# Optimization experiments

Measured on AMD Instinct MI355X. Metric: run time of the kernel, lower is better.

The kernel has to match this reference:

```python
import jax, jax.numpy as jnp
import numpy as np

N_NODES = 50000
N_EDGES = 800000
IN_DIM = 128
HID_DIM = 128
N_CLASSES = 40


def setup_inputs() -> dict:
    key = jax.random.key(0)
    ks = jax.random.split(key, 12)
    s = 0.05
    inp = {
        "X": jax.random.normal(ks[0], (N_NODES, IN_DIM), jnp.float32),
        "A": jax.random.randint(ks[1], (2, N_EDGES), 0, N_NODES, dtype=jnp.int64),
        "W0": jax.random.normal(ks[2], (HID_DIM, IN_DIM), jnp.float32) * s,
        "b0": jnp.zeros((HID_DIM,), jnp.float32),
        "W1": jax.random.normal(ks[3], (HID_DIM, HID_DIM), jnp.float32) * s,
        "b1": jnp.zeros((HID_DIM,), jnp.float32),
        "W2": jax.random.normal(ks[4], (HID_DIM, HID_DIM), jnp.float32) * s,
        "b2": jnp.zeros((HID_DIM,), jnp.float32),
        "W3": jax.random.normal(ks[5], (HID_DIM, HID_DIM), jnp.float32) * s,
        "b3": jnp.zeros((HID_DIM,), jnp.float32),
        "Wf": jax.random.normal(ks[6], (N_CLASSES, HID_DIM), jnp.float32) * s,
        "bf": jnp.zeros((N_CLASSES,), jnp.float32),
    }
    return inp


def _gcn_conv(x, W, b, src, dst):
    # FrobeniusNormGCNConv: normalize weight by Frobenius norm, then standard GCNConv
    Wn = W / jnp.linalg.norm(W)
    h = x @ Wn.T  # [N, out]
    # gcn_norm with self-loops (edge weight 1.0): deg over targets + 1 self loop
    ones = jnp.ones((dst.shape[0],), h.dtype)
    deg = jax.ops.segment_sum(ones, dst, num_segments=N_NODES) + 1.0
    dinv = jax.lax.rsqrt(deg)  # [N]
    norm = dinv[src] * dinv[dst]  # [E]
    # scatter-add of normalized source messages into targets
    agg = jax.ops.segment_sum(norm[:, None] * h[src], dst, num_segments=N_NODES)
    # self-loop contribution: dinv[i]^2 * h[i]; bias added after aggregation
    return agg + (dinv * dinv)[:, None] * h + b


def reference(X, A, W0, b0, W1, b1, W2, b2, W3, b3, Wf, bf):
    src, dst = A[0], A[1]
    h = _gcn_conv(X, W0, b0, src, dst)
    skip = h
    for W, b in ((W1, b1), (W2, b2), (W3, b3)):
        h = _gcn_conv(h, W, b, src, dst)
        h = jax.nn.relu(h)
        h = h + skip  # residual skip (dropout identity in eval mode)
        skip = h
    return h @ Wf.T + bf
```

## Files before the change

### kernel.cpp

```cpp
#include <hip/hip_runtime.h>

#define N_NODES_C 50000
#define N_EDGES_C 800000
#define DIM 128
#define NCLS 40
#define NBUK 32
#define BCAP 32768
#define NOCT 16

typedef __attribute__((ext_vector_type(8))) short bf16x8;
typedef __attribute__((ext_vector_type(4))) float f32x4;

__device__ inline float bf2f(unsigned short u) {
    union { unsigned int i; float f; } c;
    c.i = ((unsigned int)u) << 16;
    return c.f;
}
__device__ inline unsigned short f2bf(float f) {
    union { float f; unsigned int i; } c;
    c.f = f;
    unsigned int x = c.i;
    x += 0x7fffu + ((x >> 16) & 1u);
    return (unsigned short)(x >> 16);
}
__device__ inline void unp8(const uint4& g, float* f) {
    f[0] = __uint_as_float(g.x << 16); f[1] = __uint_as_float(g.x & 0xFFFF0000u);
    f[2] = __uint_as_float(g.y << 16); f[3] = __uint_as_float(g.y & 0xFFFF0000u);
    f[4] = __uint_as_float(g.z << 16); f[5] = __uint_as_float(g.z & 0xFFFF0000u);
    f[6] = __uint_as_float(g.w << 16); f[7] = __uint_as_float(g.w & 0xFFFF0000u);
}

__global__ __launch_bounds__(256) void k_pre(const float* __restrict__ W0,
                                             const float* __restrict__ W1,
                                             const float* __restrict__ W2,
                                             const float* __restrict__ W3,
                                             const float* __restrict__ Wf,
                                             unsigned short* __restrict__ Wb,
                                             unsigned short* __restrict__ Wfb,
                                             float* __restrict__ scale_inv,
                                             int* __restrict__ gcount) {
    int b = blockIdx.x;
    if (b < 64) {
        int m = b >> 4;
        int idx = (b & 15) * 256 + threadIdx.x;
        const float* W = m == 0 ? W0 : m == 1 ? W1 : m == 2 ? W2 : W3;
        float4 v = reinterpret_cast<const float4*>(W)[idx];
        reinterpret_cast<ushort4*>(Wb + (size_t)m * DIM * DIM)[idx] =
            make_ushort4(f2bf(v.x), f2bf(v.y), f2bf(v.z), f2bf(v.w));
        return;
    }
    b -= 64;
    if (b < 5) {
        int idx = b * 256 + threadIdx.x;
        float4 v = reinterpret_cast<const float4*>(Wf)[idx];
        reinterpret_cast<ushort4*>(Wfb)[idx] =
            make_ushort4(f2bf(v.x), f2bf(v.y), f2bf(v.z), f2bf(v.w));
        return;
    }
    b -= 5;
    if (b == 0 && threadIdx.x < NBUK) gcount[threadIdx.x] = 0;
    const float* W = b == 0 ? W0 : b == 1 ? W1 : b == 2 ? W2 : W3;
    float s = 0.f;
    for (int i = threadIdx.x; i < DIM * DIM; i += 256) {
        float v = W[i];
        s += v * v;
    }
    #pragma unroll
    for (int off = 32; off >= 1; off >>= 1) s += __shfl_down(s, off);
    __shared__ float red[4];
    int lane = threadIdx.x & 63, wid = threadIdx.x >> 6;
    if (lane == 0) red[wid] = s;
    __syncthreads();
    if (threadIdx.x == 0) {
        float tot = red[0] + red[1] + red[2] + red[3];
        scale_inv[b] = 1.0f / sqrtf(tot);
    }
}

__global__ __launch_bounds__(256) void k_bucket(const int* __restrict__ A,
                                                int* __restrict__ gcount,
                                                unsigned int* __restrict__ ebuk, int E) {
    __shared__ int cnt[NBUK];
    __shared__ int gbase[NBUK];
    int tid = threadIdx.x;
    if (tid < NBUK) cnt[tid] = 0;
    __syncthreads();
    int e0 = blockIdx.x * 1024;
    int s[4], d[4], b[4], r[4];
    #pragma unroll
    for (int j = 0; j < 4; ++j) {
        int e = e0 + j * 256 + tid;
        if (e < E) {
            s[j] = A[e];
            d[j] = A[E + e];
            b[j] = (int)(((unsigned long long)(unsigned)d[j] * NBUK) / N_NODES_C);
            r[j] = atomicAdd(&cnt[b[j]], 1);
        } else {
            b[j] = -1;
        }
    }
    __syncthreads();
    if (tid < NBUK) gbase[tid] = atomicAdd(&gcount[tid], cnt[tid]);
    __syncthreads();
    #pragma unroll
    for (int j = 0; j < 4; ++j) {
        if (b[j] >= 0) {
            int pos = gbase[b[j]] + r[j];
            if (pos < BCAP)
                ebuk[(size_t)b[j] * BCAP + pos] =
                    ((unsigned)d[j] << 16) | (unsigned)s[j];
        }
    }
}

__global__ __launch_bounds__(512) void k_csr(const unsigned int* __restrict__ ebuk,
                                             const int* __restrict__ gcount,
                                             int* __restrict__ ptr,
                                             float* __restrict__ dinv,
                                             unsigned short* __restrict__ esrc) {
    __shared__ unsigned int dlo[NOCT / 2][1568];
    __shared__ int gc[NBUK];
    __shared__ int wsum2[8], wpre2[8];
    int k = blockIdx.x;
    int tid = threadIdx.x;
    int base = (k * N_NODES_C + NBUK - 1) / NBUK;
    int next = ((k + 1) * N_NODES_C + NBUK - 1) / NBUK;
    int sz = next - base;

    for (int i = tid; i < (NOCT / 2) * 1568; i += 512) (&dlo[0][0])[i] = 0;
    if (tid < NBUK) gc[tid] = min(gcount[tid], BCAP);
    __syncthreads();

    int count = gc[k];
    int bucket_base = 0;
    #pragma unroll
    for (int j = 0; j < NBUK; ++j) bucket_base += (j < k) ? gc[j] : 0;
    const unsigned int* eb = ebuk + (size_t)k * BCAP;

    for (int i = tid; i < count; i += 512) {
        unsigned v = eb[i];
        int d = (int)(v >> 16) - base;
        int src = (int)(v & 0xFFFFu);
        int oct = (src * NOCT) / N_NODES_C;
        atomicAdd(&dlo[oct >> 1][d], 1u << ((oct & 1) * 16));
    }
    __syncthreads();

    int degloc[4];
    int mysum = 0;
    #pragma unroll
    for (int c = 0; c < 4; ++c) {
        int i = tid * 4 + c;
        int ds = 0;
        if (i < sz) {
            #pragma unroll
            for (int p = 0; p < NOCT / 2; ++p) {
                unsigned v = dlo[p][i];
                ds += (int)(v & 0xFFFFu) + (int)(v >> 16);
            }
        }
        degloc[c] = ds;
        mysum += ds;
    }
    int lane = tid & 63, wid = tid >> 6;
    int sc = mysum;
    #pragma unroll
    for (int off = 1; off < 64; off <<= 1) {
        int t = __shfl_up(sc, off);
        if (lane >= off) sc += t;
    }
    if (lane == 63) wsum2[wid] = sc;
    __syncthreads();
    if (tid == 0) {
        int a = 0;
        #pragma unroll
        for (int w = 0; w < 8; ++w) { wpre2[w] = a; a += wsum2[w]; }
    }
    __syncthreads();
    int run = wpre2[wid] + sc - mysum;
    #pragma unroll
    for (int c = 0; c < 4; ++c) {
        int i = tid * 4 + c;
        if (i < sz) {
            ptr[base + i] = bucket_base + run;
            dinv[base + i] = rsqrtf((float)degloc[c] + 1.0f);
            int r = run;
            #pragma unroll
            for (int p = 0; p < NOCT / 2; ++p) {
                unsigned v = dlo[p][i];
                int lo = (int)(v & 0xFFFFu), hi = (int)(v >> 16);
                dlo[p][i] = (unsigned)r | ((unsigned)(r + lo) << 16);
                r += lo + hi;
            }
            run += degloc[c];
        }
    }
    if (k == NBUK - 1 && tid == 511) ptr[N_NODES_C] = bucket_base + run;
    __syncthreads();

    for (int i = tid; i < count; i += 512) {
        unsigned v = eb[i];
        int d = (int)(v >> 16) - base;
        int src = (int)(v & 0xFFFFu);
        int oct = (src * NOCT) / N_NODES_C;
        unsigned old = atomicAdd(&dlo[oct >> 1][d], 1u << ((oct & 1) * 16));
        int pos = (int)((old >> ((oct & 1) * 16)) & 0xFFFFu);
        esrc[bucket_base + pos] = (unsigned short)src;
    }
}

template <bool F32A>
__global__ __launch_bounds__(256) void k_gemm_mfma(const void* __restrict__ Xp,
                                                   const unsigned short* __restrict__ Wb,
                                                   const float* __restrict__ scale_ptr,
                                                   const float* __restrict__ dinv,
                                                   unsigned short* __restrict__ Gb, int N) {
    int tid = threadIdx.x;
    int w = tid >> 6;
    int l = tid & 63;
    int l15 = l & 15;
    int lg = l >> 4;
    int arow = blockIdx.x * 64 + w * 16 + l15;
    if (arow >= N) arow = N - 1;
    float scale = scale_ptr[0];

    f32x4 acc[8];
    #pragma unroll
    for (int ct = 0; ct < 8; ++ct) acc[ct] = f32x4{0.f, 0.f, 0.f, 0.f};

    #pragma unroll
    for (int kc = 0; kc < 4; ++kc) {
        int ko = kc * 32 + lg * 8;
        bf16x8 a;
        if (F32A) {
            const float4* xf = reinterpret_cast<const float4*>(
                (const float*)Xp + (size_t)arow * DIM + ko);
            float4 u = xf[0], v = xf[1];
            a[0] = (short)f2bf(u.x); a[1] = (short)f2bf(u.y);
            a[2] = (short)f2bf(u.z); a[3] = (short)f2bf(u.w);
            a[4] = (short)f2bf(v.x); a[5] = (short)f2bf(v.y);
            a[6] = (short)f2bf(v.z); a[7] = (short)f2bf(v.w);
        } else {
            a = *reinterpret_cast<const bf16x8*>(
                (const unsigned short*)Xp + (size_t)arow * DIM + ko);
        }
        #pragma unroll
        for (int ct = 0; ct < 8; ++ct) {
            bf16x8 b = *reinterpret_cast<const bf16x8*>(&Wb[(size_t)(ct * 16 + l15) * DIM + ko]);
            acc[ct] = __builtin_amdgcn_mfma_f32_16x16x32_bf16(a, b, acc[ct], 0, 0, 0);
        }
    }
    int outrow0 = blockIdx.x * 64 + w * 16 + lg * 4;
    #pragma unroll
    for (int r = 0; r < 4; ++r) {
        int row = outrow0 + r;
        if (row < N) {
            float dv = dinv[row] * scale;
            #pragma unroll
            for (int ct = 0; ct < 8; ++ct)
                Gb[(size_t)row * DIM + ct * 16 + l15] = f2bf(acc[ct][r] * dv);
        }
    }
}

template <bool RELU>
__global__ __launch_bounds__(256) void k_agg(const unsigned short* __restrict__ Gb,
                                             const float* __restrict__ bias,
                                             const float* __restrict__ dinv,
                                             const int* __restrict__ ptr,
                                             const unsigned short* __restrict__ esrc,
                                             const unsigned short* __restrict__ skipb,
                                             unsigned short* __restrict__ outb) {
    int orig = blockIdx.x;
    int xcd = orig & 7;
    int idx = orig >> 3;
    int wgid = (xcd < 4 ? xcd * 1563 : 4 * 1563 + (xcd - 4) * 1562) + idx;

    int n = wgid * 4 + (threadIdx.x >> 6);
    int l = threadIdx.x & 63;
    int grp = l >> 4, li = l & 15;
    const uint4* __restrict__ Gv = reinterpret_cast<const uint4*>(Gb);
    int beg = ptr[n], end = ptr[n + 1];

    uint4 gu = Gv[(size_t)n * 16 + li];
    uint4 su;
    if (RELU) su = reinterpret_cast<const uint4*>(skipb)[(size_t)n * 16 + li];
    const float4* b4p = reinterpret_cast<const float4*>(bias);
    float4 ba = b4p[li * 2], bb = b4p[li * 2 + 1];
    float di = dinv[n];

    float acc[8] = {};
    float t[8];
    int e = beg;
    for (; e + 16 <= end; e += 16) {
        int s0 = esrc[e + grp];
        int s1 = esrc[e + 4 + grp];
        int s2 = esrc[e + 8 + grp];
        int s3 = esrc[e + 12 + grp];
        uint4 g0 = Gv[(size_t)s0 * 16 + li];
        uint4 g1 = Gv[(size_t)s1 * 16 + li];
        uint4 g2 = Gv[(size_t)s2 * 16 + li];
        uint4 g3 = Gv[(size_t)s3 * 16 + li];
        unp8(g0, t);
        #pragma unroll
        for (int j = 0; j < 8; ++j) acc[j] += t[j];
        unp8(g1, t);
        #pragma unroll
        for (int j = 0; j < 8; ++j) acc[j] += t[j];
        unp8(g2, t);
        #pragma unroll
        for (int j = 0; j < 8; ++j) acc[j] += t[j];
        unp8(g3, t);
        #pragma unroll
        for (int j = 0; j < 8; ++j) acc[j] += t[j];
    }
    for (; e + 4 <= end; e += 4) {
        int s0 = esrc[e + grp];
        uint4 g0 = Gv[(size_t)s0 * 16 + li];
        unp8(g0, t);
        #pragma unroll
        for (int j = 0; j < 8; ++j) acc[j] += t[j];
    }
    int rem = end - e;
    if (grp < rem) {
        int s0 = esrc[e + grp];
        uint4 g0 = Gv[(size_t)s0 * 16 + li];
        unp8(g0, t);
        #pragma unroll
        for (int j = 0; j < 8; ++j) acc[j] += t[j];
    }
    #pragma unroll
    for (int j = 0; j < 8; ++j) {
        acc[j] += __shfl_xor(acc[j], 16);
        acc[j] += __shfl_xor(acc[j], 32);
    }
    if (grp == 0) {
        float gs[8];
        unp8(gu, gs);
        float bv[8] = {ba.x, ba.y, ba.z, ba.w, bb.x, bb.y, bb.z, bb.w};
        float v[8];
        #pragma unroll
        for (int j = 0; j < 8; ++j) v[j] = fmaf(di, acc[j] + gs[j], bv[j]);
        if (RELU) {
            float ss[8];
            unp8(su, ss);
            #pragma unroll
            for (int j = 0; j < 8; ++j) v[j] = fmaxf(v[j], 0.f) + ss[j];
        }
        uint4 o;
        o.x = (unsigned)f2bf(v[0]) | ((unsigned)f2bf(v[1]) << 16);
        o.y = (unsigned)f2bf(v[2]) | ((unsigned)f2bf(v[3]) << 16);
        o.z = (unsigned)f2bf(v[4]) | ((unsigned)f2bf(v[5]) << 16);
        o.w = (unsigned)f2bf(v[6]) | ((unsigned)f2bf(v[7]) << 16);
        reinterpret_cast<uint4*>(outb)[(size_t)n * 16 + li] = o;
    }
}

__global__ __launch_bounds__(256) void k_final(const unsigned short* __restrict__ Hb,
                                               const unsigned short* __restrict__ Wfb,
                                               const float* __restrict__ bf,
                                               float* __restrict__ out, int N) {
    int tid = threadIdx.x;
    int w = tid >> 6;
    int l = tid & 63;
    int l15 = l & 15;
    int lg = l >> 4;
    int arow = blockIdx.x * 64 + w * 16 + l15;
    if (arow >= N) arow = N - 1;

    f32x4 acc[3];
    #pragma unroll
    for (int ct = 0; ct < 3; ++ct) acc[ct] = f32x4{0.f, 0.f, 0.f, 0.f};

    #pragma unroll
    for (int kc = 0; kc < 4; ++kc) {
        int ko = kc * 32 + lg * 8;
        bf16x8 a = *reinterpret_cast<const bf16x8*>(&Hb[(size_t)arow * DIM + ko]);
        #pragma unroll
        for (int ct = 0; ct < 3; ++ct) {
            int wr = ct * 16 + l15;
            if (wr >= NCLS) wr = 0;
            bf16x8 b = *reinterpret_cast<const bf16x8*>(&Wfb[(size_t)wr * DIM + ko]);
            acc[ct] = __builtin_amdgcn_mfma_f32_16x16x32_bf16(a, b, acc[ct], 0, 0, 0);
        }
    }
    int outrow0 = blockIdx.x * 64 + w * 16 + lg * 4;
    #pragma unroll
    for (int ct = 0; ct < 3; ++ct) {
        int c = ct * 16 + l15;
        if (c < NCLS) {
            float bias = bf[c];
            #pragma unroll
            for (int r = 0; r < 4; ++r) {
                int row = outrow0 + r;
                if (row < N) out[(size_t)row * NCLS + c] = acc[ct][r] + bias;
            }
        }
    }
}

extern "C" void kernel_launch(void* const* d_in, const int* in_sizes, int n_in,
                              void* d_out, int out_size, void* d_ws, size_t ws_size,
                              hipStream_t stream) {
    (void)in_sizes; (void)n_in; (void)out_size; (void)ws_size;
    const float* X  = (const float*)d_in[0];
    const int*   A  = (const int*)d_in[1];
    const float* W0 = (const float*)d_in[2];
    const float* b0 = (const float*)d_in[3];
    const float* W1 = (const float*)d_in[4];
    const float* b1 = (const float*)d_in[5];
    const float* W2 = (const float*)d_in[6];
    const float* b2 = (const float*)d_in[7];
    const float* W3 = (const float*)d_in[8];
    const float* b3 = (const float*)d_in[9];
    const float* Wf = (const float*)d_in[10];
    const float* bf = (const float*)d_in[11];
    float* out = (float*)d_out;

    char* base_ws = (char*)d_ws;
    size_t off = 0;
    auto alloc = [&](size_t bytes) -> char* {
        char* p = base_ws + off;
        off = (off + bytes + 255) & ~(size_t)255;
        return p;
    };
    float* scale_inv = (float*)alloc(4 * sizeof(float));
    int*   ptr    = (int*)alloc((N_NODES_C + 1) * sizeof(int));
    float* dinv   = (float*)alloc(N_NODES_C * sizeof(float));
    int*   gcount = (int*)alloc(NBUK * sizeof(int));
    unsigned int*   ebuk = (unsigned int*)alloc((size_t)NBUK * BCAP * sizeof(unsigned int));
    unsigned short* esrc = (unsigned short*)alloc((size_t)N_EDGES_C * sizeof(unsigned short));
    unsigned short* Gb  = (unsigned short*)alloc((size_t)N_NODES_C * DIM * sizeof(unsigned short));
    unsigned short* Hb1 = (unsigned short*)alloc((size_t)N_NODES_C * DIM * sizeof(unsigned short));
    unsigned short* Hb2 = (unsigned short*)alloc((size_t)N_NODES_C * DIM * sizeof(unsigned short));
    unsigned short* Wb  = (unsigned short*)alloc((size_t)4 * DIM * DIM * sizeof(unsigned short));
    unsigned short* Wfb = (unsigned short*)alloc((size_t)NCLS * DIM * sizeof(unsigned short));

    k_pre<<<73, 256, 0, stream>>>(W0, W1, W2, W3, Wf, Wb, Wfb, scale_inv, gcount);
    k_bucket<<<(N_EDGES_C + 1023) / 1024, 256, 0, stream>>>(A, gcount, ebuk, N_EDGES_C);
    k_csr<<<NBUK, 512, 0, stream>>>(ebuk, gcount, ptr, dinv, esrc);

    const int gemm_grid = (N_NODES_C + 63) / 64;
    const int agg_grid  = N_NODES_C / 4;

    k_gemm_mfma<true><<<gemm_grid, 256, 0, stream>>>(X, Wb + 0 * DIM * DIM, scale_inv + 0, dinv, Gb, N_NODES_C);
    k_agg<false><<<agg_grid, 256, 0, stream>>>(Gb, b0, dinv, ptr, esrc, nullptr, Hb1);
    k_gemm_mfma<false><<<gemm_grid, 256, 0, stream>>>(Hb1, Wb + 1 * DIM * DIM, scale_inv + 1, dinv, Gb, N_NODES_C);
    k_agg<true><<<agg_grid, 256, 0, stream>>>(Gb, b1, dinv, ptr, esrc, Hb1, Hb2);
    k_gemm_mfma<false><<<gemm_grid, 256, 0, stream>>>(Hb2, Wb + 2 * DIM * DIM, scale_inv + 2, dinv, Gb, N_NODES_C);
    k_agg<true><<<agg_grid, 256, 0, stream>>>(Gb, b2, dinv, ptr, esrc, Hb2, Hb1);
    k_gemm_mfma<false><<<gemm_grid, 256, 0, stream>>>(Hb1, Wb + 3 * DIM * DIM, scale_inv + 3, dinv, Gb, N_NODES_C);
    k_agg<true><<<agg_grid, 256, 0, stream>>>(Gb, b3, dinv, ptr, esrc, Hb1, Hb2);
    k_final<<<(N_NODES_C + 63) / 64, 256, 0, stream>>>(Hb2, Wfb, bf, out, N_NODES_C);
}
```

Baseline: 299.1 us.

## Pad per-node edge lists to multiples of 16 with zero-row sentinel

Each node's CSR edge list is padded up to a multiple of 16 entries, and the padding points at an extra all-zero row appended to the feature buffer. Each bucket now gets a fixed slab, so the cross-bucket prefix sum is no longer needed. The pointer array packs the start offset together with the 16-wide iteration count. The aggregation kernel then runs a single uniform unrolled loop with no 4-wide or remainder tails. The cost is extra gathers of the zero row, about 7.5 padded entries per node on average, which adds memory traffic that is likely cached. It also assumes no node has a degree above 4080 and that each bucket's padded edges fit in its slab.

```diff
diff --git a/kernel.cpp b/kernel.cpp
--- a/kernel.cpp
+++ b/kernel.cpp
@@ -7,6 +7,8 @@
 #define NBUK 32
 #define BCAP 32768
 #define NOCT 16
+#define SLAB 57344
+#define ZROW N_NODES_C
 
 typedef __attribute__((ext_vector_type(8))) short bf16x8;
 typedef __attribute__((ext_vector_type(4))) float f32x4;
@@ -38,7 +40,8 @@
                                              unsigned short* __restrict__ Wb,
                                              unsigned short* __restrict__ Wfb,
                                              float* __restrict__ scale_inv,
-                                             int* __restrict__ gcount) {
+                                             int* __restrict__ gcount,
+                                             unsigned short* __restrict__ Gb) {
     int b = blockIdx.x;
     if (b < 64) {
         int m = b >> 4;
@@ -58,6 +61,12 @@
         return;
     }
     b -= 5;
+    if (b == 4) {
+        if (threadIdx.x < DIM / 4)
+            reinterpret_cast<ushort4*>(Gb + (size_t)ZROW * DIM)[threadIdx.x] =
+                make_ushort4(0, 0, 0, 0);
+        return;
+    }
     if (b == 0 && threadIdx.x < NBUK) gcount[threadIdx.x] = 0;
     const float* W = b == 0 ? W0 : b == 1 ? W1 : b == 2 ? W2 : W3;
     float s = 0.f;
@@ -119,7 +128,6 @@
                                              float* __restrict__ dinv,
                                              unsigned short* __restrict__ esrc) {
     __shared__ unsigned int dlo[NOCT / 2][1568];
-    __shared__ int gc[NBUK];
     __shared__ int wsum2[8], wpre2[8];
     int k = blockIdx.x;
     int tid = threadIdx.x;
@@ -128,13 +136,10 @@
     int sz = next - base;
 
     for (int i = tid; i < (NOCT / 2) * 1568; i += 512) (&dlo[0][0])[i] = 0;
-    if (tid < NBUK) gc[tid] = min(gcount[tid], BCAP);
-    __syncthreads();
-
-    int count = gc[k];
-    int bucket_base = 0;
-    #pragma unroll
-    for (int j = 0; j < NBUK; ++j) bucket_base += (j < k) ? gc[j] : 0;
+    __syncthreads();
+
+    int count = min(gcount[k], BCAP);
+    int bucket_base = k * SLAB;
     const unsigned int* eb = ebuk + (size_t)k * BCAP;
 
     for (int i = tid; i < count; i += 512) {
@@ -146,7 +151,7 @@
     }
     __syncthreads();
 
-    int degloc[4];
+    int degloc[4], degp[4];
     int mysum = 0;
     #pragma unroll
     for (int c = 0; c < 4; ++c) {
@@ -160,7 +165,8 @@
             }
         }
         degloc[c] = ds;
-        mysum += ds;
+        degp[c] = (i < sz) ? ((ds + 15) & ~15) : 0;
+        mysum += degp[c];
     }
     int lane = tid & 63, wid = tid >> 6;
     int sc = mysum;
@@ -182,7 +188,7 @@
     for (int c = 0; c < 4; ++c) {
         int i = tid * 4 + c;
         if (i < sz) {
-            ptr[base + i] = bucket_base + run;
+            ptr[base + i] = ((bucket_base + run) << 8) | (degp[c] >> 4);
             dinv[base + i] = rsqrtf((float)degloc[c] + 1.0f);
             int r = run;
             #pragma unroll
@@ -192,10 +198,11 @@
                 dlo[p][i] = (unsigned)r | ((unsigned)(r + lo) << 16);
                 r += lo + hi;
             }
-            run += degloc[c];
-        }
-    }
-    if (k == NBUK - 1 && tid == 511) ptr[N_NODES_C] = bucket_base + run;
+            for (int j = degloc[c]; j < degp[c]; ++j)
+                esrc[bucket_base + run + j] = (unsigned short)ZROW;
+            run += degp[c];
+        }
+    }
     __syncthreads();
 
     for (int i = tid; i < count; i += 512) {
@@ -280,7 +287,9 @@
     int l = threadIdx.x & 63;
     int grp = l >> 4, li = l & 15;
     const uint4* __restrict__ Gv = reinterpret_cast<const uint4*>(Gb);
-    int beg = ptr[n], end = ptr[n + 1];
+    int p = ptr[n];
+    int beg = p >> 8;
+    int niter = p & 255;
 
     uint4 gu = Gv[(size_t)n * 16 + li];
     uint4 su;
@@ -291,8 +300,8 @@
 
     float acc[8] = {};
     float t[8];
-    int e = beg;
-    for (; e + 16 <= end; e += 16) {
+    for (int it = 0; it < niter; ++it) {
+        int e = beg + it * 16;
         int s0 = esrc[e + grp];
         int s1 = esrc[e + 4 + grp];
         int s2 = esrc[e + 8 + grp];
@@ -311,21 +320,6 @@
         #pragma unroll
         for (int j = 0; j < 8; ++j) acc[j] += t[j];
         unp8(g3, t);
-        #pragma unroll
-        for (int j = 0; j < 8; ++j) acc[j] += t[j];
-    }
-    for (; e + 4 <= end; e += 4) {
-        int s0 = esrc[e + grp];
-        uint4 g0 = Gv[(size_t)s0 * 16 + li];
-        unp8(g0, t);
-        #pragma unroll
-        for (int j = 0; j < 8; ++j) acc[j] += t[j];
-    }
-    int rem = end - e;
-    if (grp < rem) {
-        int s0 = esrc[e + grp];
-        uint4 g0 = Gv[(size_t)s0 * 16 + li];
-        unp8(g0, t);
         #pragma unroll
         for (int j = 0; j < 8; ++j) acc[j] += t[j];
     }
@@ -425,18 +419,18 @@
         return p;
     };
     float* scale_inv = (float*)alloc(4 * sizeof(float));
-    int*   ptr    = (int*)alloc((N_NODES_C + 1) * sizeof(int));
+    int*   ptr    = (int*)alloc(N_NODES_C * sizeof(int));
     float* dinv   = (float*)alloc(N_NODES_C * sizeof(float));
     int*   gcount = (int*)alloc(NBUK * sizeof(int));
     unsigned int*   ebuk = (unsigned int*)alloc((size_t)NBUK * BCAP * sizeof(unsigned int));
-    unsigned short* esrc = (unsigned short*)alloc((size_t)N_EDGES_C * sizeof(unsigned short));
-    unsigned short* Gb  = (unsigned short*)alloc((size_t)N_NODES_C * DIM * sizeof(unsigned short));
+    unsigned short* esrc = (unsigned short*)alloc((size_t)NBUK * SLAB * sizeof(unsigned short));
+    unsigned short* Gb  = (unsigned short*)alloc((size_t)(N_NODES_C + 1) * DIM * sizeof(unsigned short));
     unsigned short* Hb1 = (unsigned short*)alloc((size_t)N_NODES_C * DIM * sizeof(unsigned short));
     unsigned short* Hb2 = (unsigned short*)alloc((size_t)N_NODES_C * DIM * sizeof(unsigned short));
     unsigned short* Wb  = (unsigned short*)alloc((size_t)4 * DIM * DIM * sizeof(unsigned short));
     unsigned short* Wfb = (unsigned short*)alloc((size_t)NCLS * DIM * sizeof(unsigned short));
 
-    k_pre<<<73, 256, 0, stream>>>(W0, W1, W2, W3, Wf, Wb, Wfb, scale_inv, gcount);
+    k_pre<<<74, 256, 0, stream>>>(W0, W1, W2, W3, Wf, Wb, Wfb, scale_inv, gcount, Gb);
     k_bucket<<<(N_EDGES_C + 1023) / 1024, 256, 0, stream>>>(A, gcount, ebuk, N_EDGES_C);
     k_csr<<<NBUK, 512, 0, stream>>>(ebuk, gcount, ptr, dinv, esrc);
 
```

Result: no change. 293.5 us (median of 3 runs) (-1.9%).
